# Kernel tuning notes

Hardware: AMD Instinct MI355X
Metric: run time of the kernel (lower is better)

The kernel has to match this reference:

```python
import jax, jax.numpy as jnp
import numpy as np

N = 100000
D = 64
E = 1600000
EPS = 1e-5


def setup_inputs() -> dict:
    key = jax.random.key(0)
    k1, k2, k3, k4, k5, k6 = jax.random.split(key, 6)
    node_features = jax.random.normal(k1, (N, D), dtype=jnp.float32)
    edge_index = jax.random.randint(k2, (E, 2), 0, N, dtype=jnp.int64)
    # torch Linear params: W [out, in], b [out]
    lim_m = 1.0 / np.sqrt(2 * D)
    W_msg = jax.random.uniform(k3, (D, 2 * D), minval=-lim_m, maxval=lim_m, dtype=jnp.float32)
    b_msg = jax.random.uniform(k4, (D,), minval=-lim_m, maxval=lim_m, dtype=jnp.float32)
    W_upd = jax.random.uniform(k5, (D, 2 * D), minval=-lim_m, maxval=lim_m, dtype=jnp.float32)
    b_upd = jax.random.uniform(k6, (D,), minval=-lim_m, maxval=lim_m, dtype=jnp.float32)
    gamma = jnp.ones((D,), dtype=jnp.float32)
    beta = jnp.zeros((D,), dtype=jnp.float32)
    return {
        "node_features": node_features,
        "edge_index": edge_index,
        "W_msg": W_msg,
        "b_msg": b_msg,
        "W_upd": W_upd,
        "b_upd": b_upd,
        "gamma": gamma,
        "beta": beta,
    }


def _layer_norm(x, gamma, beta):
    mu = jnp.mean(x, axis=-1, keepdims=True)
    var = jnp.mean(jnp.square(x - mu), axis=-1, keepdims=True)
    return (x - mu) * jax.lax.rsqrt(var + EPS) * gamma + beta


def reference(node_features, edge_index, W_msg, b_msg, W_upd, b_upd, gamma, beta):
    src = edge_index[:, 0]
    tgt = edge_index[:, 1]
    # per-edge message: relu(Linear(cat(x[src], x[tgt])))  -- split weight to avoid [E,2D] concat
    Wm_s = W_msg[:, :D]  # [D, D] applied to src feats
    Wm_t = W_msg[:, D:]  # [D, D] applied to tgt feats
    msg = jax.nn.relu(node_features[src] @ Wm_s.T + node_features[tgt] @ Wm_t.T + b_msg)  # [E, D]
    # scatter-mean into target nodes
    messages = jax.ops.segment_sum(msg, tgt, num_segments=N)  # [N, D]
    counts = jax.ops.segment_sum(jnp.ones((edge_index.shape[0],), dtype=node_features.dtype), tgt, num_segments=N)
    counts = jnp.maximum(counts, 1.0)[:, None]
    messages = messages / counts
    # update: relu(Linear(cat(x, messages))) + residual + LayerNorm
    Wu_x = W_upd[:, :D]
    Wu_m = W_upd[:, D:]
    updated = jax.nn.relu(node_features @ Wu_x.T + messages @ Wu_m.T + b_upd)
    return _layer_norm(updated + node_features, gamma, beta)
```

## Files before the change

kernel.cpp:

```cpp
#include <hip/hip_runtime.h>
#include <hip/hip_bf16.h>
#include <stdint.h>

#define NNODES 100000
#define DF 64
#define NEDGES 1600000
#define ND (NNODES * DF)
#define BKT 100
#define NBUCK 1000
#define CHUNK 128
#define NCHUNK (NEDGES / CHUNK)
#define NPW 25

static __device__ __forceinline__ float bf2f(unsigned short u) {
    union { uint32_t i; float f; } c; c.i = ((uint32_t)u) << 16; return c.f;
}
static __device__ __forceinline__ unsigned short f2bf(float f) {
    union { __hip_bfloat16 b; unsigned short u; } c; c.b = __float2bfloat16(f); return c.u;
}
static __device__ __forceinline__ void unpack2(uint32_t u, float& lo, float& hi) {
    union { uint32_t i; float f; } a, b;
    a.i = u << 16; b.i = u & 0xFFFF0000u;
    lo = a.f; hi = b.f;
}

__global__ void detect_k(const unsigned short* __restrict__ x,
                         const unsigned int* __restrict__ ei,
                         int* __restrict__ flags) {
    __shared__ int cnt_sane, cnt_odd_nz;
    if (threadIdx.x == 0) { cnt_sane = 0; cnt_odd_nz = 0; }
    __syncthreads();
    unsigned short s = x[threadIdx.x * 2];
    unsigned short m = s & 0x7FFF;
    if (m < 0x0080 || (m >= 0x3000 && m <= 0x4200)) atomicAdd(&cnt_sane, 1);
    if (threadIdx.x < 64) {
        if (ei[threadIdx.x * 2 + 1] != 0u) atomicAdd(&cnt_odd_nz, 1);
    }
    __syncthreads();
    if (threadIdx.x == 0) {
        flags[0] = (cnt_sane >= 192) ? 1 : 0;
        flags[1] = (cnt_odd_nz == 0) ? 1 : 0;
    }
}

__global__ void wconv_k(const int* __restrict__ flags,
                        const void* __restrict__ Wm, const void* __restrict__ Wu,
                        const void* __restrict__ bm, const void* __restrict__ bu,
                        const void* __restrict__ ga, const void* __restrict__ be,
                        float* __restrict__ WfMT, float* __restrict__ WfUT,
                        float* __restrict__ prm) {
    const int bf = flags[0];
    int i = blockIdx.x * 256 + threadIdx.x;
    if (i < 16384) {
        const void* src = (i < 8192) ? Wm : Wu;
        float* dst = (i < 8192) ? WfMT : WfUT;
        int ii = i & 8191, j = ii >> 6, k = ii & 63;
        int si = (j & 63) * 128 + ((j >> 6) ? 64 : 0) + k;
        float v = bf ? bf2f(((const unsigned short*)src)[si]) : ((const float*)src)[si];
        dst[(j >> 6) * 4096 + k * 64 + (j & 63)] = v;
    } else if (i < 16384 + 320) {
        int t = i - 16384, which = t >> 6, k = t & 63;
        if (which == 4) { prm[t] = 0.f; }
        else {
            const void* p = (which == 0) ? bm : (which == 1) ? bu : (which == 2) ? ga : be;
            prm[t] = bf ? bf2f(((const unsigned short*)p)[k]) : ((const float*)p)[k];
        }
    }
}

__global__ __launch_bounds__(256, 1) void mm_k(const int* __restrict__ flags,
                                               const void* __restrict__ xv,
                                               const float* __restrict__ WT,
                                               const float* __restrict__ bias,
                                               void* __restrict__ outv,
                                               int of) {
    const int lane = threadIdx.x & 63;
    const int wib = __builtin_amdgcn_readfirstlane(threadIdx.x >> 6);
    const int bf = flags[0];

    float w[64];
    #pragma unroll
    for (int k = 0; k < 64; ++k) w[k] = WT[k * 64 + lane];
    const float bs = bias[lane];

    const int wv = blockIdx.x * 4 + wib;
    const int n0 = wv * NPW;
    if (n0 >= NNODES) return;
    const int n1 = (n0 + NPW < NNODES) ? n0 + NPW : NNODES;
    for (int n = n0; n < n1; ++n) {
        float a0 = 0.f, a1 = 0.f, a2 = 0.f, a3 = 0.f;
        if (bf) {
            const uint4* xr = (const uint4*)((const unsigned short*)xv + (size_t)n * DF);
            #pragma unroll
            for (int q = 0; q < 8; ++q) {
                uint4 v = xr[q];
                float x0,x1,x2,x3,x4,x5,x6,x7;
                unpack2(v.x, x0, x1); unpack2(v.y, x2, x3);
                unpack2(v.z, x4, x5); unpack2(v.w, x6, x7);
                a0 = fmaf(x0, w[8*q+0], a0); a1 = fmaf(x1, w[8*q+1], a1);
                a2 = fmaf(x2, w[8*q+2], a2); a3 = fmaf(x3, w[8*q+3], a3);
                a0 = fmaf(x4, w[8*q+4], a0); a1 = fmaf(x5, w[8*q+5], a1);
                a2 = fmaf(x6, w[8*q+6], a2); a3 = fmaf(x7, w[8*q+7], a3);
            }
        } else {
            const float4* xr = (const float4*)((const float*)xv + (size_t)n * DF);
            #pragma unroll
            for (int q = 0; q < 16; ++q) {
                float4 v = xr[q];
                a0 = fmaf(v.x, w[4*q+0], a0); a1 = fmaf(v.y, w[4*q+1], a1);
                a2 = fmaf(v.z, w[4*q+2], a2); a3 = fmaf(v.w, w[4*q+3], a3);
            }
        }
        float r = (a0 + a1) + (a2 + a3) + bs;
        size_t gi = (size_t)n * DF + lane;
        if (of) ((float*)outv)[gi] = r;
        else    ((unsigned short*)outv)[gi] = f2bf(r);
    }
}

__global__ __launch_bounds__(256) void bhist_k(const int* __restrict__ flags,
                                               const int* __restrict__ ei,
                                               int* __restrict__ BktCnt) {
    __shared__ int h[NBUCK];
    const int i64 = flags[1];
    for (int i = threadIdx.x; i < NBUCK; i += 256) h[i] = 0;
    __syncthreads();
    int stride = gridDim.x * 256;
    for (int e = blockIdx.x * 256 + threadIdx.x; e < NEDGES; e += stride) {
        int tgt = i64 ? ei[4*e + 2] : ei[2*e + 1];
        if ((unsigned)tgt < NNODES) atomicAdd(&h[tgt / BKT], 1);
    }
    __syncthreads();
    for (int b = threadIdx.x; b < NBUCK; b += 256)
        if (h[b]) atomicAdd(BktCnt + b, h[b]);
}

__global__ __launch_bounds__(1024) void bscan_k(const int* __restrict__ BktCnt,
                                                int* __restrict__ BktOff,
                                                int* __restrict__ BktCur) {
    __shared__ int lds[1024];
    int t = threadIdx.x;
    int c = (t < NBUCK) ? BktCnt[t] : 0;
    lds[t] = c;
    __syncthreads();
    for (int off = 1; off < 1024; off <<= 1) {
        int add = (t >= off) ? lds[t - off] : 0;
        __syncthreads();
        lds[t] += add;
        __syncthreads();
    }
    if (t < NBUCK) {
        int ex = lds[t] - c;
        BktOff[t] = ex;
        BktCur[t] = ex;
    }
    if (t == NBUCK - 1) BktOff[NBUCK] = lds[t];
}

__global__ __launch_bounds__(256) void bfill_k(const int* __restrict__ flags,
                                               const int* __restrict__ ei,
                                               int* __restrict__ BktCur,
                                               int* __restrict__ BktE) {
    __shared__ int h[NBUCK], h2[NBUCK], basee[NBUCK];
    const int i64 = flags[1];
    for (int i = threadIdx.x; i < NBUCK; i += 256) { h[i] = 0; h2[i] = 0; }
    __syncthreads();
    const int stride = gridDim.x * 256;
    for (int e = blockIdx.x * 256 + threadIdx.x; e < NEDGES; e += stride) {
        int tgt = i64 ? ei[4*e + 2] : ei[2*e + 1];
        if ((unsigned)tgt < NNODES) atomicAdd(&h[tgt / BKT], 1);
    }
    __syncthreads();
    for (int b = threadIdx.x; b < NBUCK; b += 256)
        if (h[b]) basee[b] = atomicAdd(BktCur + b, h[b]);
    __syncthreads();
    for (int e = blockIdx.x * 256 + threadIdx.x; e < NEDGES; e += stride) {
        int src, tgt;
        if (i64) { src = ei[4*e]; tgt = ei[4*e + 2]; }
        else     { src = ei[2*e]; tgt = ei[2*e + 1]; }
        if ((unsigned)tgt >= NNODES) continue;
        int b = tgt / BKT;
        int tl = tgt - b * BKT;
        int r = atomicAdd(&h2[b], 1);
        BktE[basee[b] + r] = (tl << 24) | (src & 0xFFFFFF);
    }
}

__global__ __launch_bounds__(256) void tsort_k(const int* __restrict__ BktOff,
                                               const int* __restrict__ BktE,
                                               int* __restrict__ CsrSrc,
                                               int* __restrict__ Row) {
    __shared__ int oc[128], excl[128], cur[128];
    const int tid = threadIdx.x;
    const int b = blockIdx.x;
    const int s = BktOff[b], e = BktOff[b + 1];
    const int n = e - s;
    if (tid < 128) { oc[tid] = 0; }
    __syncthreads();
    for (int i = tid; i < n; i += 256)
        atomicAdd(&oc[((unsigned)BktE[s + i]) >> 24], 1);
    __syncthreads();
    if (tid < 128) excl[tid] = (tid > 0) ? oc[tid - 1] : 0;
    __syncthreads();
    for (int off = 1; off < 128; off <<= 1) {
        int add = (tid >= off && tid < 128) ? excl[tid - off] : 0;
        __syncthreads();
        if (tid < 128) excl[tid] += add;
        __syncthreads();
    }
    if (tid < BKT) {
        Row[b * BKT + tid] = s + excl[tid];
        cur[tid] = excl[tid];
    }
    if (b == 0 && tid == 0) Row[NNODES] = NEDGES;
    __syncthreads();
    for (int i = tid; i < n; i += 256) {
        int v = BktE[s + i];
        int tl = ((unsigned)v) >> 24;
        int p = atomicAdd(&cur[tl], 1);
        int sv = v & 0xFFFFFF;
        if (sv >= NNODES) sv = 0;
        CsrSrc[s + p] = sv << 6;
    }
}

__global__ __launch_bounds__(256) void cstart_k(const int* __restrict__ Row,
                                                int* __restrict__ ChunkT) {
    int c = blockIdx.x * 256 + threadIdx.x;
    if (c > NCHUNK) return;
    if (c == NCHUNK) { ChunkT[NCHUNK] = NNODES; return; }
    int target = c * CHUNK;
    int lo = 0, hi = NNODES + 1;
    while (lo < hi) { int mid = (lo + hi) >> 1; if (Row[mid] >= target) hi = mid; else lo = mid + 1; }
    ChunkT[c] = lo;
}

__global__ __launch_bounds__(256) void agg_k(const unsigned short* __restrict__ Ps,
                                             const unsigned short* __restrict__ Pt,
                                             const int* __restrict__ Row,
                                             const int* __restrict__ CsrSrc,
                                             const int* __restrict__ ChunkT,
                                             unsigned short* __restrict__ Msg) {
    const int lane = threadIdx.x & 63;
    const int wib = __builtin_amdgcn_readfirstlane(threadIdx.x >> 6);
    const int w = blockIdx.x * 4 + wib;
    if (w >= NCHUNK) return;

    const int t_lo = ChunkT[w];
    const int t_hi = ChunkT[w + 1];
    if (t_lo >= t_hi) return;

    int segS = Row[t_lo];
    for (int t = t_lo; t < t_hi; ++t) {
        const int segE = Row[t + 1];
        const int deg = segE - segS;
        float ptv = bf2f(Pt[(size_t)t * DF + lane]);
        float pa0 = 0.f, pa1 = 0.f, pa2 = 0.f, pa3 = 0.f;
        for (int i = segS; i < segE; i += 16) {
            #pragma unroll
            for (int j = 0; j < 16; ++j) {
                const int idx = i + j;
                const int ok = idx < segE;
                const int sv = CsrSrc[ok ? idx : segS];
                float p = bf2f(Ps[(size_t)(unsigned)sv + lane]);
                float v = ok ? fmaxf(p + ptv, 0.f) : 0.f;
                if ((j & 3) == 0)      pa0 += v;
                else if ((j & 3) == 1) pa1 += v;
                else if ((j & 3) == 2) pa2 += v;
                else                   pa3 += v;
            }
        }
        float macc = (pa0 + pa1) + (pa2 + pa3);
        float mval = (deg > 0) ? (macc / (float)deg) : 0.f;
        Msg[(size_t)t * DF + lane] = f2bf(mval);
        segS = segE;
    }
}

__global__ __launch_bounds__(256, 1) void u2_k(const int* __restrict__ flags,
                                               const void* __restrict__ xv,
                                               const unsigned short* __restrict__ Msg,
                                               const float* __restrict__ t1,
                                               const float* __restrict__ WT,
                                               const float* __restrict__ prm,
                                               void* __restrict__ outv) {
    const int lane = threadIdx.x & 63;
    const int wib = __builtin_amdgcn_readfirstlane(threadIdx.x >> 6);
    const int bf = flags[0];

    float w[64];
    #pragma unroll
    for (int k = 0; k < 64; ++k) w[k] = WT[k * 64 + lane];
    const float ga = prm[128 + lane];
    const float be = prm[192 + lane];

    const unsigned short* x16 = (const unsigned short*)xv;
    const float* xf = (const float*)xv;

    const int wv = blockIdx.x * 4 + wib;
    const int n0 = wv * NPW;
    if (n0 >= NNODES) return;
    const int n1 = (n0 + NPW < NNODES) ? n0 + NPW : NNODES;
    for (int n = n0; n < n1; ++n) {
        float b0 = 0.f, b1 = 0.f, b2 = 0.f, b3 = 0.f;
        const uint4* mw = (const uint4*)(Msg + (size_t)n * DF);
        #pragma unroll
        for (int q = 0; q < 8; ++q) {
            uint4 v = mw[q];
            float m0,m1,m2,m3,m4,m5,m6,m7;
            unpack2(v.x, m0, m1); unpack2(v.y, m2, m3);
            unpack2(v.z, m4, m5); unpack2(v.w, m6, m7);
            b0 = fmaf(m0, w[8*q+0], b0); b1 = fmaf(m1, w[8*q+1], b1);
            b2 = fmaf(m2, w[8*q+2], b2); b3 = fmaf(m3, w[8*q+3], b3);
            b0 = fmaf(m4, w[8*q+4], b0); b1 = fmaf(m5, w[8*q+5], b1);
            b2 = fmaf(m6, w[8*q+6], b2); b3 = fmaf(m7, w[8*q+7], b3);
        }
        size_t gi = (size_t)n * DF + lane;
        float t  = t1[gi];
        float xl = bf ? bf2f(x16[gi]) : xf[gi];
        float u = fmaxf((b0 + b1) + (b2 + b3) + t, 0.f);
        float r = u + xl;

        float s = r, s2 = r * r;
        #pragma unroll
        for (int m = 1; m < 64; m <<= 1) {
            s  += __shfl_xor(s, m, 64);
            s2 += __shfl_xor(s2, m, 64);
        }
        float mu  = s * (1.0f / 64.0f);
        float var = fmaxf(s2 * (1.0f / 64.0f) - mu * mu, 0.f);
        float o = (r - mu) * rsqrtf(var + 1e-5f) * ga + be;

        if (bf) ((__hip_bfloat16*)outv)[gi] = __float2bfloat16(o);
        else    ((float*)outv)[gi] = o;
    }
}

extern "C" void kernel_launch(void* const* d_in, const int* in_sizes, int n_in,
                              void* d_out, int out_size, void* d_ws, size_t ws_size,
                              hipStream_t stream) {
    const void* x  = d_in[0];
    const int*  ei = (const int*)d_in[1];
    const void* Wm = d_in[2];
    const void* bm = d_in[3];
    const void* Wu = d_in[4];
    const void* bu = d_in[5];
    const void* ga = d_in[6];
    const void* be = d_in[7];

    char* ws = (char*)d_ws;
    size_t off = 0;
    unsigned short* Ps  = (unsigned short*)(ws + off); off += (size_t)ND * 2;
    unsigned short* Pt  = (unsigned short*)(ws + off); off += (size_t)ND * 2;
    unsigned short* Msg = (unsigned short*)(ws + off); off += (size_t)ND * 2;
    int*   BktE   = (int*)(ws + off); off += (size_t)NEDGES * 4;
    int*   CsrSrc = (int*)(ws + off); off += (size_t)NEDGES * 4;
    int*   Row    = (int*)(ws + off); off += (size_t)(NNODES + 1) * 4;
    int*   BktCnt = (int*)(ws + off); off += NBUCK * 4;
    int*   BktOff = (int*)(ws + off); off += (NBUCK + 1) * 4;
    int*   BktCur = (int*)(ws + off); off += NBUCK * 4;
    int*   flg    = (int*)(ws + off); off += 16;
    float* WfMT   = (float*)(ws + off); off += 8192 * 4;
    float* WfUT   = (float*)(ws + off); off += 8192 * 4;
    float* prm    = (float*)(ws + off); off += 320 * 4;

    float* t1 = (float*)Ps;
    int* ChunkT = BktE;

    (void)hipMemsetAsync(BktCnt, 0, NBUCK * 4, stream);

    detect_k<<<1, 256, 0, stream>>>((const unsigned short*)x, (const unsigned int*)ei, flg);
    wconv_k<<<66, 256, 0, stream>>>(flg, Wm, Wu, bm, bu, ga, be, WfMT, WfUT, prm);

    mm_k<<<1024, 256, 0, stream>>>(flg, x, WfMT,        prm + 256, Ps, 0);
    mm_k<<<1024, 256, 0, stream>>>(flg, x, WfMT + 4096, prm,       Pt, 0);

    bhist_k<<<256, 256, 0, stream>>>(flg, ei, BktCnt);
    bscan_k<<<1, 1024, 0, stream>>>(BktCnt, BktOff, BktCur);
    bfill_k<<<128, 256, 0, stream>>>(flg, ei, BktCur, BktE);
    tsort_k<<<NBUCK, 256, 0, stream>>>(BktOff, BktE, CsrSrc, Row);

    cstart_k<<<(NCHUNK + 256) / 256, 256, 0, stream>>>(Row, ChunkT);

    agg_k<<<(NCHUNK + 3) / 4, 256, 0, stream>>>(Ps, Pt, Row, CsrSrc, ChunkT, Msg);

    mm_k<<<1024, 256, 0, stream>>>(flg, x, WfUT, prm + 64, t1, 1);

    u2_k<<<1024, 256, 0, stream>>>(flg, x, Msg, t1, WfUT + 4096, prm, d_out);
}
```

Before: 331.4 us.

## Fuse paired node projections and update matmuls into single kernels

Merges the two source/target projection launches into one kernel in which two waves per block compute the Ps projection and two compute Pt for the same nodes, so each x row is read by both roles at about the same time. The update path is fused too: one wave pair computes x·Wu_x while the other computes Msg·Wu_m, they exchange partial sums through double-buffered shared memory, and the LayerNorm is applied directly. This drops the fp32 t1 intermediate round trip and two launches. The cost is a block-wide barrier per node and half as many node-processing waves per block, offset by raising nodes per wave from 25 to 49.

```diff
diff --git a/kernel.cpp b/kernel.cpp
--- a/kernel.cpp
+++ b/kernel.cpp
@@ -10,7 +10,7 @@
 #define NBUCK 1000
 #define CHUNK 128
 #define NCHUNK (NEDGES / CHUNK)
-#define NPW 25
+#define NPW 49
 
 static __device__ __forceinline__ float bf2f(unsigned short u) {
     union { uint32_t i; float f; } c; c.i = ((uint32_t)u) << 16; return c.f;
@@ -68,22 +68,26 @@
     }
 }
 
-__global__ __launch_bounds__(256, 1) void mm_k(const int* __restrict__ flags,
-                                               const void* __restrict__ xv,
-                                               const float* __restrict__ WT,
-                                               const float* __restrict__ bias,
-                                               void* __restrict__ outv,
-                                               int of) {
+__global__ __launch_bounds__(256, 1) void proj2_k(const int* __restrict__ flags,
+                                                  const void* __restrict__ xv,
+                                                  const float* __restrict__ WfMT,
+                                                  const float* __restrict__ prm,
+                                                  unsigned short* __restrict__ Ps,
+                                                  unsigned short* __restrict__ Pt) {
     const int lane = threadIdx.x & 63;
     const int wib = __builtin_amdgcn_readfirstlane(threadIdx.x >> 6);
+    const int role = wib >> 1;
+    const int slot = wib & 1;
     const int bf = flags[0];
 
+    const float* wbase = WfMT + (role ? 4096 : 0);
     float w[64];
     #pragma unroll
-    for (int k = 0; k < 64; ++k) w[k] = WT[k * 64 + lane];
-    const float bs = bias[lane];
-
-    const int wv = blockIdx.x * 4 + wib;
+    for (int k = 0; k < 64; ++k) w[k] = wbase[k * 64 + lane];
+    const float bias = role ? prm[lane] : 0.f;
+    unsigned short* outp = role ? Pt : Ps;
+
+    const int wv = blockIdx.x * 2 + slot;
     const int n0 = wv * NPW;
     if (n0 >= NNODES) return;
     const int n1 = (n0 + NPW < NNODES) ? n0 + NPW : NNODES;
@@ -111,10 +115,7 @@
                 a2 = fmaf(v.z, w[4*q+2], a2); a3 = fmaf(v.w, w[4*q+3], a3);
             }
         }
-        float r = (a0 + a1) + (a2 + a3) + bs;
-        size_t gi = (size_t)n * DF + lane;
-        if (of) ((float*)outv)[gi] = r;
-        else    ((unsigned short*)outv)[gi] = f2bf(r);
+        outp[(size_t)n * DF + lane] = f2bf((a0 + a1) + (a2 + a3) + bias);
     }
 }
 
@@ -277,62 +278,99 @@
     }
 }
 
-__global__ __launch_bounds__(256, 1) void u2_k(const int* __restrict__ flags,
-                                               const void* __restrict__ xv,
-                                               const unsigned short* __restrict__ Msg,
-                                               const float* __restrict__ t1,
-                                               const float* __restrict__ WT,
-                                               const float* __restrict__ prm,
-                                               void* __restrict__ outv) {
+__global__ __launch_bounds__(256, 1) void upd2_k(const int* __restrict__ flags,
+                                                 const void* __restrict__ xv,
+                                                 const unsigned short* __restrict__ Msg,
+                                                 const float* __restrict__ WfUT,
+                                                 const float* __restrict__ prm,
+                                                 void* __restrict__ outv) {
+    __shared__ float bb[2][2][64];
     const int lane = threadIdx.x & 63;
     const int wib = __builtin_amdgcn_readfirstlane(threadIdx.x >> 6);
+    const int role = wib >> 1;
+    const int slot = wib & 1;
     const int bf = flags[0];
 
+    const float* wbase = WfUT + (role ? 4096 : 0);
     float w[64];
     #pragma unroll
-    for (int k = 0; k < 64; ++k) w[k] = WT[k * 64 + lane];
+    for (int k = 0; k < 64; ++k) w[k] = wbase[k * 64 + lane];
+    const float bu = prm[64 + lane];
     const float ga = prm[128 + lane];
     const float be = prm[192 + lane];
 
     const unsigned short* x16 = (const unsigned short*)xv;
     const float* xf = (const float*)xv;
 
-    const int wv = blockIdx.x * 4 + wib;
+    const int wv = blockIdx.x * 2 + slot;
     const int n0 = wv * NPW;
-    if (n0 >= NNODES) return;
-    const int n1 = (n0 + NPW < NNODES) ? n0 + NPW : NNODES;
-    for (int n = n0; n < n1; ++n) {
-        float b0 = 0.f, b1 = 0.f, b2 = 0.f, b3 = 0.f;
-        const uint4* mw = (const uint4*)(Msg + (size_t)n * DF);
-        #pragma unroll
-        for (int q = 0; q < 8; ++q) {
-            uint4 v = mw[q];
-            float m0,m1,m2,m3,m4,m5,m6,m7;
-            unpack2(v.x, m0, m1); unpack2(v.y, m2, m3);
-            unpack2(v.z, m4, m5); unpack2(v.w, m6, m7);
-            b0 = fmaf(m0, w[8*q+0], b0); b1 = fmaf(m1, w[8*q+1], b1);
-            b2 = fmaf(m2, w[8*q+2], b2); b3 = fmaf(m3, w[8*q+3], b3);
-            b0 = fmaf(m4, w[8*q+4], b0); b1 = fmaf(m5, w[8*q+5], b1);
-            b2 = fmaf(m6, w[8*q+6], b2); b3 = fmaf(m7, w[8*q+7], b3);
+    int c = 0;
+    for (int i = 0; i < NPW; ++i) {
+        const int n = n0 + i;
+        const bool valid = n < NNODES;
+        float a0 = 0.f, a1 = 0.f, a2 = 0.f, a3 = 0.f;
+        float xl = 0.f;
+        if (valid) {
+            if (role) {
+                const uint4* mw = (const uint4*)(Msg + (size_t)n * DF);
+                #pragma unroll
+                for (int q = 0; q < 8; ++q) {
+                    uint4 v = mw[q];
+                    float m0,m1,m2,m3,m4,m5,m6,m7;
+                    unpack2(v.x, m0, m1); unpack2(v.y, m2, m3);
+                    unpack2(v.z, m4, m5); unpack2(v.w, m6, m7);
+                    a0 = fmaf(m0, w[8*q+0], a0); a1 = fmaf(m1, w[8*q+1], a1);
+                    a2 = fmaf(m2, w[8*q+2], a2); a3 = fmaf(m3, w[8*q+3], a3);
+                    a0 = fmaf(m4, w[8*q+4], a0); a1 = fmaf(m5, w[8*q+5], a1);
+                    a2 = fmaf(m6, w[8*q+6], a2); a3 = fmaf(m7, w[8*q+7], a3);
+                }
+                bb[c][slot][lane] = (a0 + a1) + (a2 + a3);
+            } else {
+                if (bf) {
+                    const uint4* xr = (const uint4*)(x16 + (size_t)n * DF);
+                    #pragma unroll
+                    for (int q = 0; q < 8; ++q) {
+                        uint4 v = xr[q];
+                        float x0,x1,x2,x3,x4,x5,x6,x7;
+                        unpack2(v.x, x0, x1); unpack2(v.y, x2, x3);
+                        unpack2(v.z, x4, x5); unpack2(v.w, x6, x7);
+                        a0 = fmaf(x0, w[8*q+0], a0); a1 = fmaf(x1, w[8*q+1], a1);
+                        a2 = fmaf(x2, w[8*q+2], a2); a3 = fmaf(x3, w[8*q+3], a3);
+                        a0 = fmaf(x4, w[8*q+4], a0); a1 = fmaf(x5, w[8*q+5], a1);
+                        a2 = fmaf(x6, w[8*q+6], a2); a3 = fmaf(x7, w[8*q+7], a3);
+                    }
+                    xl = bf2f(x16[(size_t)n * DF + lane]);
+                } else {
+                    const float4* xr = (const float4*)(xf + (size_t)n * DF);
+                    #pragma unroll
+                    for (int q = 0; q < 16; ++q) {
+                        float4 v = xr[q];
+                        a0 = fmaf(v.x, w[4*q+0], a0); a1 = fmaf(v.y, w[4*q+1], a1);
+                        a2 = fmaf(v.z, w[4*q+2], a2); a3 = fmaf(v.w, w[4*q+3], a3);
+                    }
+                    xl = xf[(size_t)n * DF + lane];
+                }
+            }
         }
-        size_t gi = (size_t)n * DF + lane;
-        float t  = t1[gi];
-        float xl = bf ? bf2f(x16[gi]) : xf[gi];
-        float u = fmaxf((b0 + b1) + (b2 + b3) + t, 0.f);
-        float r = u + xl;
-
-        float s = r, s2 = r * r;
-        #pragma unroll
-        for (int m = 1; m < 64; m <<= 1) {
-            s  += __shfl_xor(s, m, 64);
-            s2 += __shfl_xor(s2, m, 64);
+        __syncthreads();
+        if (!role && valid) {
+            float b = bb[c][slot][lane];
+            float u = fmaxf((a0 + a1) + (a2 + a3) + b + bu, 0.f);
+            float r = u + xl;
+            float s = r, s2 = r * r;
+            #pragma unroll
+            for (int m = 1; m < 64; m <<= 1) {
+                s  += __shfl_xor(s, m, 64);
+                s2 += __shfl_xor(s2, m, 64);
+            }
+            float mu  = s * (1.0f / 64.0f);
+            float var = fmaxf(s2 * (1.0f / 64.0f) - mu * mu, 0.f);
+            float o = (r - mu) * rsqrtf(var + 1e-5f) * ga + be;
+            size_t gi = (size_t)n * DF + lane;
+            if (bf) ((__hip_bfloat16*)outv)[gi] = __float2bfloat16(o);
+            else    ((float*)outv)[gi] = o;
         }
-        float mu  = s * (1.0f / 64.0f);
-        float var = fmaxf(s2 * (1.0f / 64.0f) - mu * mu, 0.f);
-        float o = (r - mu) * rsqrtf(var + 1e-5f) * ga + be;
-
-        if (bf) ((__hip_bfloat16*)outv)[gi] = __float2bfloat16(o);
-        else    ((float*)outv)[gi] = o;
+        c ^= 1;
     }
 }
 
@@ -364,7 +402,6 @@
     float* WfUT   = (float*)(ws + off); off += 8192 * 4;
     float* prm    = (float*)(ws + off); off += 320 * 4;
 
-    float* t1 = (float*)Ps;
     int* ChunkT = BktE;
 
     (void)hipMemsetAsync(BktCnt, 0, NBUCK * 4, stream);
@@ -372,8 +409,7 @@
     detect_k<<<1, 256, 0, stream>>>((const unsigned short*)x, (const unsigned int*)ei, flg);
     wconv_k<<<66, 256, 0, stream>>>(flg, Wm, Wu, bm, bu, ga, be, WfMT, WfUT, prm);
 
-    mm_k<<<1024, 256, 0, stream>>>(flg, x, WfMT,        prm + 256, Ps, 0);
-    mm_k<<<1024, 256, 0, stream>>>(flg, x, WfMT + 4096, prm,       Pt, 0);
+    proj2_k<<<1024, 256, 0, stream>>>(flg, x, WfMT, prm, Ps, Pt);
 
     bhist_k<<<256, 256, 0, stream>>>(flg, ei, BktCnt);
     bscan_k<<<1, 1024, 0, stream>>>(BktCnt, BktOff, BktCur);
@@ -384,7 +420,5 @@
 
     agg_k<<<(NCHUNK + 3) / 4, 256, 0, stream>>>(Ps, Pt, Row, CsrSrc, ChunkT, Msg);
 
-    mm_k<<<1024, 256, 0, stream>>>(flg, x, WfUT, prm + 64, t1, 1);
-
-    u2_k<<<1024, 256, 0, stream>>>(flg, x, Msg, t1, WfUT + 4096, prm, d_out);
-}
+    upd2_k<<<1024, 256, 0, stream>>>(flg, x, Msg, WfUT, prm, d_out);
+}
```

After: 356.2 us. +7.5%, slower.

## Replace two-level bucket sort CSR build with per-node global atomic counting sort

Applied to the files above, without the earlier changes.

Merges the format-detection kernel into the weight-conversion kernel, saving one launch. Replaces the bucketed histogram/scan/fill/in-bucket sort pipeline with a direct per-target-node counting sort: a global-atomic histogram over 100k nodes, a single-block scan, and a fill pass using global atomics on per-node cursors. This drops the intermediate BktE buffer and one kernel, but adds heavy global atomic contention, a serial single-block scan over 100k entries, and scattered writes. Edge order within a node now depends on atomic ordering, so float summation order can vary between runs.

```diff
diff --git a/kernel.cpp b/kernel.cpp
--- a/kernel.cpp
+++ b/kernel.cpp
@@ -6,11 +6,10 @@
 #define DF 64
 #define NEDGES 1600000
 #define ND (NNODES * DF)
-#define BKT 100
-#define NBUCK 1000
 #define CHUNK 128
 #define NCHUNK (NEDGES / CHUNK)
 #define NPW 25
+#define SPT 98
 
 static __device__ __forceinline__ float bf2f(unsigned short u) {
     union { uint32_t i; float f; } c; c.i = ((uint32_t)u) << 16; return c.f;
@@ -24,32 +23,30 @@
     lo = a.f; hi = b.f;
 }
 
-__global__ void detect_k(const unsigned short* __restrict__ x,
-                         const unsigned int* __restrict__ ei,
-                         int* __restrict__ flags) {
-    __shared__ int cnt_sane, cnt_odd_nz;
-    if (threadIdx.x == 0) { cnt_sane = 0; cnt_odd_nz = 0; }
-    __syncthreads();
-    unsigned short s = x[threadIdx.x * 2];
-    unsigned short m = s & 0x7FFF;
-    if (m < 0x0080 || (m >= 0x3000 && m <= 0x4200)) atomicAdd(&cnt_sane, 1);
-    if (threadIdx.x < 64) {
-        if (ei[threadIdx.x * 2 + 1] != 0u) atomicAdd(&cnt_odd_nz, 1);
-    }
-    __syncthreads();
-    if (threadIdx.x == 0) {
-        flags[0] = (cnt_sane >= 192) ? 1 : 0;
-        flags[1] = (cnt_odd_nz == 0) ? 1 : 0;
-    }
-}
-
-__global__ void wconv_k(const int* __restrict__ flags,
+__global__ void wconv_k(const unsigned short* __restrict__ x,
+                        const unsigned int* __restrict__ eiu,
                         const void* __restrict__ Wm, const void* __restrict__ Wu,
                         const void* __restrict__ bm, const void* __restrict__ bu,
                         const void* __restrict__ ga, const void* __restrict__ be,
                         float* __restrict__ WfMT, float* __restrict__ WfUT,
-                        float* __restrict__ prm) {
-    const int bf = flags[0];
+                        float* __restrict__ prm, int* __restrict__ flags) {
+    __shared__ int cnt_sane, cnt_odd_nz;
+    if (threadIdx.x == 0) { cnt_sane = 0; cnt_odd_nz = 0; }
+    __syncthreads();
+    {
+        unsigned short s = x[threadIdx.x * 2];
+        unsigned short m = s & 0x7FFF;
+        if (m < 0x0080 || (m >= 0x3000 && m <= 0x4200)) atomicAdd(&cnt_sane, 1);
+        if (threadIdx.x < 64) {
+            if (eiu[threadIdx.x * 2 + 1] != 0u) atomicAdd(&cnt_odd_nz, 1);
+        }
+    }
+    __syncthreads();
+    const int bf = (cnt_sane >= 192) ? 1 : 0;
+    if (blockIdx.x == 0 && threadIdx.x == 0) {
+        flags[0] = bf;
+        flags[1] = (cnt_odd_nz == 0) ? 1 : 0;
+    }
     int i = blockIdx.x * 256 + threadIdx.x;
     if (i < 16384) {
         const void* src = (i < 8192) ? Wm : Wu;
@@ -118,109 +115,62 @@
     }
 }
 
-__global__ __launch_bounds__(256) void bhist_k(const int* __restrict__ flags,
+__global__ __launch_bounds__(256) void thist_k(const int* __restrict__ flags,
                                                const int* __restrict__ ei,
-                                               int* __restrict__ BktCnt) {
-    __shared__ int h[NBUCK];
+                                               int* __restrict__ Cnt) {
     const int i64 = flags[1];
-    for (int i = threadIdx.x; i < NBUCK; i += 256) h[i] = 0;
-    __syncthreads();
-    int stride = gridDim.x * 256;
-    for (int e = blockIdx.x * 256 + threadIdx.x; e < NEDGES; e += stride) {
-        int tgt = i64 ? ei[4*e + 2] : ei[2*e + 1];
-        if ((unsigned)tgt < NNODES) atomicAdd(&h[tgt / BKT], 1);
-    }
-    __syncthreads();
-    for (int b = threadIdx.x; b < NBUCK; b += 256)
-        if (h[b]) atomicAdd(BktCnt + b, h[b]);
-}
-
-__global__ __launch_bounds__(1024) void bscan_k(const int* __restrict__ BktCnt,
-                                                int* __restrict__ BktOff,
-                                                int* __restrict__ BktCur) {
-    __shared__ int lds[1024];
-    int t = threadIdx.x;
-    int c = (t < NBUCK) ? BktCnt[t] : 0;
-    lds[t] = c;
-    __syncthreads();
-    for (int off = 1; off < 1024; off <<= 1) {
-        int add = (t >= off) ? lds[t - off] : 0;
-        __syncthreads();
-        lds[t] += add;
-        __syncthreads();
-    }
-    if (t < NBUCK) {
-        int ex = lds[t] - c;
-        BktOff[t] = ex;
-        BktCur[t] = ex;
-    }
-    if (t == NBUCK - 1) BktOff[NBUCK] = lds[t];
-}
-
-__global__ __launch_bounds__(256) void bfill_k(const int* __restrict__ flags,
-                                               const int* __restrict__ ei,
-                                               int* __restrict__ BktCur,
-                                               int* __restrict__ BktE) {
-    __shared__ int h[NBUCK], h2[NBUCK], basee[NBUCK];
-    const int i64 = flags[1];
-    for (int i = threadIdx.x; i < NBUCK; i += 256) { h[i] = 0; h2[i] = 0; }
-    __syncthreads();
     const int stride = gridDim.x * 256;
     for (int e = blockIdx.x * 256 + threadIdx.x; e < NEDGES; e += stride) {
         int tgt = i64 ? ei[4*e + 2] : ei[2*e + 1];
-        if ((unsigned)tgt < NNODES) atomicAdd(&h[tgt / BKT], 1);
-    }
+        if ((unsigned)tgt < NNODES) atomicAdd(Cnt + tgt, 1);
+    }
+}
+
+__global__ __launch_bounds__(1024) void tscan_k(const int* __restrict__ Cnt,
+                                                int* __restrict__ Row,
+                                                int* __restrict__ Cur) {
+    __shared__ int ps[1024];
+    const int t = threadIdx.x;
+    const int base = t * SPT;
+    int sum = 0;
+    for (int i = 0; i < SPT; ++i) {
+        int idx = base + i;
+        sum += (idx < NNODES) ? Cnt[idx] : 0;
+    }
+    ps[t] = sum;
     __syncthreads();
-    for (int b = threadIdx.x; b < NBUCK; b += 256)
-        if (h[b]) basee[b] = atomicAdd(BktCur + b, h[b]);
-    __syncthreads();
+    for (int off = 1; off < 1024; off <<= 1) {
+        int add = (t >= off) ? ps[t - off] : 0;
+        __syncthreads();
+        ps[t] += add;
+        __syncthreads();
+    }
+    int run = ps[t] - sum;
+    for (int i = 0; i < SPT; ++i) {
+        int idx = base + i;
+        if (idx < NNODES) {
+            Row[idx] = run;
+            Cur[idx] = run;
+            run += Cnt[idx];
+        }
+    }
+    if (t == 1023) Row[NNODES] = ps[1023];
+}
+
+__global__ __launch_bounds__(256) void tfill_k(const int* __restrict__ flags,
+                                               const int* __restrict__ ei,
+                                               int* __restrict__ Cur,
+                                               int* __restrict__ CsrSrc) {
+    const int i64 = flags[1];
+    const int stride = gridDim.x * 256;
     for (int e = blockIdx.x * 256 + threadIdx.x; e < NEDGES; e += stride) {
         int src, tgt;
         if (i64) { src = ei[4*e]; tgt = ei[4*e + 2]; }
         else     { src = ei[2*e]; tgt = ei[2*e + 1]; }
         if ((unsigned)tgt >= NNODES) continue;
-        int b = tgt / BKT;
-        int tl = tgt - b * BKT;
-        int r = atomicAdd(&h2[b], 1);
-        BktE[basee[b] + r] = (tl << 24) | (src & 0xFFFFFF);
-    }
-}
-
-__global__ __launch_bounds__(256) void tsort_k(const int* __restrict__ BktOff,
-                                               const int* __restrict__ BktE,
-                                               int* __restrict__ CsrSrc,
-                                               int* __restrict__ Row) {
-    __shared__ int oc[128], excl[128], cur[128];
-    const int tid = threadIdx.x;
-    const int b = blockIdx.x;
-    const int s = BktOff[b], e = BktOff[b + 1];
-    const int n = e - s;
-    if (tid < 128) { oc[tid] = 0; }
-    __syncthreads();
-    for (int i = tid; i < n; i += 256)
-        atomicAdd(&oc[((unsigned)BktE[s + i]) >> 24], 1);
-    __syncthreads();
-    if (tid < 128) excl[tid] = (tid > 0) ? oc[tid - 1] : 0;
-    __syncthreads();
-    for (int off = 1; off < 128; off <<= 1) {
-        int add = (tid >= off && tid < 128) ? excl[tid - off] : 0;
-        __syncthreads();
-        if (tid < 128) excl[tid] += add;
-        __syncthreads();
-    }
-    if (tid < BKT) {
-        Row[b * BKT + tid] = s + excl[tid];
-        cur[tid] = excl[tid];
-    }
-    if (b == 0 && tid == 0) Row[NNODES] = NEDGES;
-    __syncthreads();
-    for (int i = tid; i < n; i += 256) {
-        int v = BktE[s + i];
-        int tl = ((unsigned)v) >> 24;
-        int p = atomicAdd(&cur[tl], 1);
-        int sv = v & 0xFFFFFF;
-        if (sv >= NNODES) sv = 0;
-        CsrSrc[s + p] = sv << 6;
+        int p = atomicAdd(Cur + tgt, 1);
+        if ((unsigned)src >= NNODES) src = 0;
+        CsrSrc[p] = src << 6;
     }
 }
 
@@ -353,32 +303,29 @@
     unsigned short* Ps  = (unsigned short*)(ws + off); off += (size_t)ND * 2;
     unsigned short* Pt  = (unsigned short*)(ws + off); off += (size_t)ND * 2;
     unsigned short* Msg = (unsigned short*)(ws + off); off += (size_t)ND * 2;
-    int*   BktE   = (int*)(ws + off); off += (size_t)NEDGES * 4;
     int*   CsrSrc = (int*)(ws + off); off += (size_t)NEDGES * 4;
     int*   Row    = (int*)(ws + off); off += (size_t)(NNODES + 1) * 4;
-    int*   BktCnt = (int*)(ws + off); off += NBUCK * 4;
-    int*   BktOff = (int*)(ws + off); off += (NBUCK + 1) * 4;
-    int*   BktCur = (int*)(ws + off); off += NBUCK * 4;
+    int*   Cnt    = (int*)(ws + off); off += (size_t)NNODES * 4;
+    int*   Cur    = (int*)(ws + off); off += (size_t)NNODES * 4;
+    int*   ChunkT = (int*)(ws + off); off += (NCHUNK + 1) * 4;
     int*   flg    = (int*)(ws + off); off += 16;
     float* WfMT   = (float*)(ws + off); off += 8192 * 4;
     float* WfUT   = (float*)(ws + off); off += 8192 * 4;
     float* prm    = (float*)(ws + off); off += 320 * 4;
 
     float* t1 = (float*)Ps;
-    int* ChunkT = BktE;
-
-    (void)hipMemsetAsync(BktCnt, 0, NBUCK * 4, stream);
-
-    detect_k<<<1, 256, 0, stream>>>((const unsigned short*)x, (const unsigned int*)ei, flg);
-    wconv_k<<<66, 256, 0, stream>>>(flg, Wm, Wu, bm, bu, ga, be, WfMT, WfUT, prm);
+
+    (void)hipMemsetAsync(Cnt, 0, (size_t)NNODES * 4, stream);
+
+    wconv_k<<<66, 256, 0, stream>>>((const unsigned short*)x, (const unsigned int*)ei,
+                                    Wm, Wu, bm, bu, ga, be, WfMT, WfUT, prm, flg);
 
     mm_k<<<1024, 256, 0, stream>>>(flg, x, WfMT,        prm + 256, Ps, 0);
     mm_k<<<1024, 256, 0, stream>>>(flg, x, WfMT + 4096, prm,       Pt, 0);
 
-    bhist_k<<<256, 256, 0, stream>>>(flg, ei, BktCnt);
-    bscan_k<<<1, 1024, 0, stream>>>(BktCnt, BktOff, BktCur);
-    bfill_k<<<128, 256, 0, stream>>>(flg, ei, BktCur, BktE);
-    tsort_k<<<NBUCK, 256, 0, stream>>>(BktOff, BktE, CsrSrc, Row);
+    thist_k<<<512, 256, 0, stream>>>(flg, ei, Cnt);
+    tscan_k<<<1, 1024, 0, stream>>>(Cnt, Row, Cur);
+    tfill_k<<<512, 256, 0, stream>>>(flg, ei, Cur, CsrSrc);
 
     cstart_k<<<(NCHUNK + 256) / 256, 256, 0, stream>>>(Row, ChunkT);
 
```

New measurement: 719.1 us. +117.0%, slower.
